# Kernel optimization log

Measured on AMD Instinct MI355X. Metric: run time of the kernel, lower is better.

The kernel has to match this reference:

```python
import jax, jax.numpy as jnp
import numpy as np

B = 2048          # batch
E = 32            # number of expert FCs (len(out_features_nested))
IN = 2048         # in_features
OUT = 1024        # out_features (uniform across experts)


def setup_inputs() -> dict:
    key = jax.random.key(0)
    k1, k2, k3, k4 = jax.random.split(key, 4)
    features = jax.random.normal(k1, (B, IN), dtype=jnp.float32)
    activated = jax.random.normal(k2, (B, E), dtype=jnp.float32)
    # Stacked per-expert Linear params: W[e] is [OUT, IN], b[e] is [OUT]
    W = jax.random.normal(k3, (E, OUT, IN), dtype=jnp.float32) * (1.0 / np.sqrt(IN))
    b = jax.random.normal(k4, (E, OUT), dtype=jnp.float32) * 0.01
    return {"features": features, "W": W, "b": b, "activated": activated, "top_k": 4}


def reference(features, W, b, activated, top_k):
    # Original: parent_indices = activated.argsort(dim=1)[:, :top_k]  (ascending!)
    idx = jnp.argsort(activated, axis=1)[:, :top_k]            # [B, K] int
    # Dense all-expert compute (grouped GEMM), then per-sample gather of the
    # top_k selected experts' outputs. Equivalent math to per-sample Linear calls.
    all_out = jnp.einsum('bi,eoi->beo', features, W) + b        # [B, E, OUT]
    out = jnp.take_along_axis(all_out, idx[:, :, None], axis=1)  # [B, K, OUT]
    return out
```

## Files before the change

kernel.cpp:

```cpp
#include <hip/hip_runtime.h>
#include <hip/hip_bf16.h>
#include <stdint.h>

#define B_N     2048
#define E_N     32
#define IN_N    2048
#define OUT_N   1024
#define TOPK    4

#define BM      256
#define BN      256
#define BK      32
#define NT      (OUT_N / BN)
#define NKT     (IN_N / BK)
#define THREADS 512
#define MAX_SLOTS 64
#define GRID_GEMM (MAX_SLOTS * NT)

#define WS_COUNTS 0
#define WS_NSLOTS 32
#define WS_DESC   64
#define WS_LISTS  256

typedef float  f32x4  __attribute__((ext_vector_type(4)));
typedef __bf16 bf16x8 __attribute__((ext_vector_type(8)));

union Pack8 { bf16x8 v; uint4 u; };

__device__ __forceinline__ uint4 pack8(f32x4 lo, f32x4 hi) {
  Pack8 p;
#pragma unroll
  for (int j = 0; j < 4; ++j) { p.v[j] = (__bf16)lo[j]; p.v[j + 4] = (__bf16)hi[j]; }
  return p.u;
}
__device__ __forceinline__ bf16x8 as_frag(uint4 u) { Pack8 p; p.u = u; return p.v; }

__global__ void k_zero(int* __restrict__ ws) {
  if (threadIdx.x < 64) ws[threadIdx.x] = 0;
}

__global__ void k_topk(const float* __restrict__ act, int* __restrict__ ws) {
  int b = blockIdx.x * blockDim.x + threadIdx.x;
  if (b >= B_N) return;
  float v[E_N];
  const float* a = act + (size_t)b * E_N;
#pragma unroll
  for (int e = 0; e < E_N; ++e) v[e] = a[e];
  unsigned chosen = 0;
#pragma unroll
  for (int k = 0; k < TOPK; ++k) {
    float mv = 3.4e38f; int mi = 0;
#pragma unroll
    for (int e = 0; e < E_N; ++e) {
      bool sel = (((chosen >> e) & 1u) == 0u) && (v[e] < mv);
      mv = sel ? v[e] : mv;
      mi = sel ? e : mi;
    }
    chosen |= (1u << mi);
    int pos = atomicAdd(&ws[WS_COUNTS + mi], 1);
    ws[WS_LISTS + mi * B_N + pos] = (b << 2) | k;
  }
}

__global__ void k_tiles(int* __restrict__ ws) {
  int e = threadIdx.x;
  int c = (e < E_N) ? ws[WS_COUNTS + e] : 0;
  int t = (c + BM - 1) / BM;
  int off = 0, tot = 0;
  for (int j = 0; j < E_N; ++j) {
    int tj = __shfl(t, j, 64);
    if (j < e) off += tj;
    tot += tj;
  }
  if (e < E_N) {
    for (int i = 0; i < t; ++i) ws[WS_DESC + off + i] = (e << 6) | i;
  }
  if (e == 0) ws[WS_NSLOTS] = tot;
}

__global__ __launch_bounds__(THREADS, 2)
void k_gemm(const float* __restrict__ feat, const float* __restrict__ Wm,
            const float* __restrict__ bias, const int* __restrict__ ws,
            float* __restrict__ out) {
  int p = blockIdx.x;
  int x = p & 7, j = p >> 3;
  int slot = x + 8 * (j >> 2);
  int nt   = j & 3;
  if (slot >= ws[WS_NSLOTS]) return;
  int desc = ws[WS_DESC + slot];
  int e = desc >> 6, mt = desc & 63;
  int count = ws[WS_COUNTS + e];
  int m0 = mt * BM;

  __shared__ uint4 lds4[4096];
  __shared__ int gids[BM];

  int tid  = threadIdx.x;
  int lane = tid & 63;
  int wv   = tid >> 6;
  int wm   = wv >> 2;
  int wn   = wv & 3;

  int seg  = tid & 3;
  int ar0  = tid >> 2;
  int ar1  = 128 + (tid >> 2);
  int gid0 = -1, gid1 = -1;
  if (m0 + ar0 < count) gid0 = ws[WS_LISTS + e * B_N + m0 + ar0];
  if (m0 + ar1 < count) gid1 = ws[WS_LISTS + e * B_N + m0 + ar1];
  if (seg == 0) { gids[ar0] = gid0; gids[ar1] = gid1; }
  const float* aptr0 = feat + (size_t)(gid0 >> 2) * IN_N + seg * 8;
  const float* aptr1 = feat + (size_t)(gid1 >> 2) * IN_N + seg * 8;
  int a_wi0 = ar0 * 4 + (seg ^ ((ar0 >> 1) & 3));
  int a_wi1 = ar1 * 4 + (seg ^ ((ar1 >> 1) & 3));

  int wr0 = tid >> 2, wr1 = 128 + (tid >> 2);
  const float* wptr0 = Wm + ((size_t)e * OUT_N + (size_t)(nt * BN + wr0)) * IN_N + seg * 8;
  const float* wptr1 = Wm + ((size_t)e * OUT_N + (size_t)(nt * BN + wr1)) * IN_N + seg * 8;
  int w_wi0 = 1024 + wr0 * 4 + (seg ^ ((wr0 >> 1) & 3));
  int w_wi1 = 1024 + wr1 * 4 + (seg ^ ((wr1 >> 1) & 3));

  int aidx[8], bidx[4];
#pragma unroll
  for (int mi = 0; mi < 8; ++mi) {
    int r = wm * 128 + mi * 16 + (lane & 15);
    aidx[mi] = r * 4 + ((lane >> 4) ^ ((r >> 1) & 3));
  }
#pragma unroll
  for (int ni = 0; ni < 4; ++ni) {
    int r = wn * 64 + ni * 16 + (lane & 15);
    bidx[ni] = 1024 + r * 4 + ((lane >> 4) ^ ((r >> 1) & 3));
  }

  f32x4 ra[4], rw[4];
  const f32x4 zero4 = {0.f, 0.f, 0.f, 0.f};

#define LOAD_TILE(K0)                                                        \
  do {                                                                       \
    if (gid0 >= 0) {                                                         \
      ra[0] = *(const f32x4*)(aptr0 + (K0));                                 \
      ra[1] = *(const f32x4*)(aptr0 + (K0) + 4);                             \
    } else { ra[0] = zero4; ra[1] = zero4; }                                 \
    if (gid1 >= 0) {                                                         \
      ra[2] = *(const f32x4*)(aptr1 + (K0));                                 \
      ra[3] = *(const f32x4*)(aptr1 + (K0) + 4);                             \
    } else { ra[2] = zero4; ra[3] = zero4; }                                 \
    rw[0] = *(const f32x4*)(wptr0 + (K0));                                   \
    rw[1] = *(const f32x4*)(wptr0 + (K0) + 4);                               \
    rw[2] = *(const f32x4*)(wptr1 + (K0));                                   \
    rw[3] = *(const f32x4*)(wptr1 + (K0) + 4);                               \
  } while (0)

#define WRITE_TILE(BUF)                                                      \
  do {                                                                       \
    lds4[(BUF) * 2048 + a_wi0] = pack8(ra[0], ra[1]);                        \
    lds4[(BUF) * 2048 + a_wi1] = pack8(ra[2], ra[3]);                        \
    lds4[(BUF) * 2048 + w_wi0] = pack8(rw[0], rw[1]);                        \
    lds4[(BUF) * 2048 + w_wi1] = pack8(rw[2], rw[3]);                        \
  } while (0)

  f32x4 acc[8][4] = {};

  LOAD_TILE(0);
  WRITE_TILE(0);
  __syncthreads();

  int cur = 0;
#pragma unroll 1
  for (int kt = 0; kt < NKT; ++kt) {
    bool pf = (kt + 1 < NKT);
    if (pf) LOAD_TILE((kt + 1) * BK);

    int base = cur * 2048;
    bf16x8 af[8], bfr[4];
#pragma unroll
    for (int mi = 0; mi < 8; ++mi) af[mi] = as_frag(lds4[base + aidx[mi]]);
#pragma unroll
    for (int ni = 0; ni < 4; ++ni) bfr[ni] = as_frag(lds4[base + bidx[ni]]);
#pragma unroll
    for (int mi = 0; mi < 8; ++mi)
#pragma unroll
      for (int ni = 0; ni < 4; ++ni)
        acc[mi][ni] = __builtin_amdgcn_mfma_f32_16x16x32_bf16(af[mi], bfr[ni], acc[mi][ni], 0, 0, 0);

    if (pf) WRITE_TILE(cur ^ 1);
    __syncthreads();
    cur ^= 1;
  }

#pragma unroll
  for (int ni = 0; ni < 4; ++ni) {
    int col = nt * BN + wn * 64 + ni * 16 + (lane & 15);
    float bs = bias[e * OUT_N + col];
#pragma unroll
    for (int mi = 0; mi < 8; ++mi) {
#pragma unroll
      for (int j2 = 0; j2 < 4; ++j2) {
        int g = gids[wm * 128 + mi * 16 + (lane >> 4) * 4 + j2];
        if (g >= 0) out[(size_t)g * OUT_N + col] = acc[mi][ni][j2] + bs;
      }
    }
  }
}

extern "C" void kernel_launch(void* const* d_in, const int* in_sizes, int n_in,
                              void* d_out, int out_size, void* d_ws, size_t ws_size,
                              hipStream_t stream) {
  const float* feat = (const float*)d_in[0];
  const float* Wm   = (const float*)d_in[1];
  const float* bias = (const float*)d_in[2];
  const float* act  = (const float*)d_in[3];
  int*   ws  = (int*)d_ws;
  float* out = (float*)d_out;

  hipLaunchKernelGGL(k_zero,  dim3(1),          dim3(64),      0, stream, ws);
  hipLaunchKernelGGL(k_topk,  dim3(B_N / 256),  dim3(256),     0, stream, act, ws);
  hipLaunchKernelGGL(k_tiles, dim3(1),          dim3(64),      0, stream, ws);
  hipLaunchKernelGGL(k_gemm,  dim3(GRID_GEMM),  dim3(THREADS), 0, stream,
                     feat, Wm, bias, ws, out);
}
```

Baseline: 154.7 us.

## Pre-convert features to bf16 and stream A tiles directly into LDS

Adds a pre-pass that converts the feature matrix to bf16 in workspace. The gathered A rows are then loaded straight into LDS with global_load_lds, which removes the register round-trip and the fp32-to-bf16 packing from the inner loop. The K loop becomes a two-step unrolled pipeline with a triple-buffered A tile, double-buffered W registers, and explicit vmcnt waits instead of __syncthreads. The cost is an extra conversion kernel and its traffic, a larger LDS footprint, and the fragility of hand-placed waitcnt and barrier ordering.

```diff
diff --git a/kernel.cpp b/kernel.cpp
--- a/kernel.cpp
+++ b/kernel.cpp
@@ -21,6 +21,7 @@
 #define WS_NSLOTS 32
 #define WS_DESC   64
 #define WS_LISTS  256
+#define FEATB_OFF 264192
 
 typedef float  f32x4  __attribute__((ext_vector_type(4)));
 typedef __bf16 bf16x8 __attribute__((ext_vector_type(8)));
@@ -35,8 +36,21 @@
 }
 __device__ __forceinline__ bf16x8 as_frag(uint4 u) { Pack8 p; p.u = u; return p.v; }
 
+__device__ __forceinline__ void glds16(const void* g, const uint4* l) {
+  __builtin_amdgcn_global_load_lds(
+      (const __attribute__((address_space(1))) void*)g,
+      (__attribute__((address_space(3))) void*)l, 16, 0, 0);
+}
+
 __global__ void k_zero(int* __restrict__ ws) {
   if (threadIdx.x < 64) ws[threadIdx.x] = 0;
+}
+
+__global__ void k_conv(const float* __restrict__ f, unsigned short* __restrict__ o) {
+  int i = (blockIdx.x * 256 + threadIdx.x) * 8;
+  f32x4 a = *(const f32x4*)(f + i);
+  f32x4 b = *(const f32x4*)(f + i + 4);
+  *(uint4*)(o + i) = pack8(a, b);
 }
 
 __global__ void k_topk(const float* __restrict__ act, int* __restrict__ ws) {
@@ -79,7 +93,7 @@
 }
 
 __global__ __launch_bounds__(THREADS, 2)
-void k_gemm(const float* __restrict__ feat, const float* __restrict__ Wm,
+void k_gemm(const unsigned short* __restrict__ featb, const float* __restrict__ Wm,
             const float* __restrict__ bias, const int* __restrict__ ws,
             float* __restrict__ out) {
   int p = blockIdx.x;
@@ -92,8 +106,7 @@
   int count = ws[WS_COUNTS + e];
   int m0 = mt * BM;
 
-  __shared__ uint4 lds4[4096];
-  __shared__ int gids[BM];
+  __shared__ uint4 lds4[5120];
 
   int tid  = threadIdx.x;
   int lane = tid & 63;
@@ -101,23 +114,22 @@
   int wm   = wv >> 2;
   int wn   = wv & 3;
 
-  int seg  = tid & 3;
-  int ar0  = tid >> 2;
-  int ar1  = 128 + (tid >> 2);
-  int gid0 = -1, gid1 = -1;
-  if (m0 + ar0 < count) gid0 = ws[WS_LISTS + e * B_N + m0 + ar0];
-  if (m0 + ar1 < count) gid1 = ws[WS_LISTS + e * B_N + m0 + ar1];
-  if (seg == 0) { gids[ar0] = gid0; gids[ar1] = gid1; }
-  const float* aptr0 = feat + (size_t)(gid0 >> 2) * IN_N + seg * 8;
-  const float* aptr1 = feat + (size_t)(gid1 >> 2) * IN_N + seg * 8;
-  int a_wi0 = ar0 * 4 + (seg ^ ((ar0 >> 1) & 3));
-  int a_wi1 = ar1 * 4 + (seg ^ ((ar1 >> 1) & 3));
-
-  int wr0 = tid >> 2, wr1 = 128 + (tid >> 2);
-  const float* wptr0 = Wm + ((size_t)e * OUT_N + (size_t)(nt * BN + wr0)) * IN_N + seg * 8;
-  const float* wptr1 = Wm + ((size_t)e * OUT_N + (size_t)(nt * BN + wr1)) * IN_N + seg * 8;
-  int w_wi0 = 1024 + wr0 * 4 + (seg ^ ((wr0 >> 1) & 3));
-  int w_wi1 = 1024 + wr1 * 4 + (seg ^ ((wr1 >> 1) & 3));
+  const unsigned short* asrc0;
+  const unsigned short* asrc1;
+  {
+    int s0 = wv * 128 + lane,      r0 = s0 >> 2, t0 = s0 & 3;
+    int s1 = wv * 128 + 64 + lane, r1 = s1 >> 2, t1 = s1 & 3;
+    int g0 = (m0 + r0 < count) ? (ws[WS_LISTS + e * B_N + m0 + r0] >> 2) : 0;
+    int g1 = (m0 + r1 < count) ? (ws[WS_LISTS + e * B_N + m0 + r1] >> 2) : 0;
+    asrc0 = featb + (size_t)g0 * IN_N + ((t0 ^ ((r0 >> 1) & 3)) * 8);
+    asrc1 = featb + (size_t)g1 * IN_N + ((t1 ^ ((r1 >> 1) & 3)) * 8);
+  }
+
+  int wrow = tid >> 1, half = tid & 1;
+  const float* wp = Wm + ((size_t)e * OUT_N + (size_t)(nt * BN + wrow)) * IN_N + half * 16;
+  int wswz = (wrow >> 1) & 3;
+  int wsl0 = wrow * 4 + ((half * 2) ^ wswz);
+  int wsl1 = wrow * 4 + ((half * 2 + 1) ^ wswz);
 
   int aidx[8], bidx[4];
 #pragma unroll
@@ -128,64 +140,94 @@
 #pragma unroll
   for (int ni = 0; ni < 4; ++ni) {
     int r = wn * 64 + ni * 16 + (lane & 15);
-    bidx[ni] = 1024 + r * 4 + ((lane >> 4) ^ ((r >> 1) & 3));
-  }
-
-  f32x4 ra[4], rw[4];
-  const f32x4 zero4 = {0.f, 0.f, 0.f, 0.f};
-
-#define LOAD_TILE(K0)                                                        \
-  do {                                                                       \
-    if (gid0 >= 0) {                                                         \
-      ra[0] = *(const f32x4*)(aptr0 + (K0));                                 \
-      ra[1] = *(const f32x4*)(aptr0 + (K0) + 4);                             \
-    } else { ra[0] = zero4; ra[1] = zero4; }                                 \
-    if (gid1 >= 0) {                                                         \
-      ra[2] = *(const f32x4*)(aptr1 + (K0));                                 \
-      ra[3] = *(const f32x4*)(aptr1 + (K0) + 4);                             \
-    } else { ra[2] = zero4; ra[3] = zero4; }                                 \
-    rw[0] = *(const f32x4*)(wptr0 + (K0));                                   \
-    rw[1] = *(const f32x4*)(wptr0 + (K0) + 4);                               \
-    rw[2] = *(const f32x4*)(wptr1 + (K0));                                   \
-    rw[3] = *(const f32x4*)(wptr1 + (K0) + 4);                               \
-  } while (0)
-
-#define WRITE_TILE(BUF)                                                      \
-  do {                                                                       \
-    lds4[(BUF) * 2048 + a_wi0] = pack8(ra[0], ra[1]);                        \
-    lds4[(BUF) * 2048 + a_wi1] = pack8(ra[2], ra[3]);                        \
-    lds4[(BUF) * 2048 + w_wi0] = pack8(rw[0], rw[1]);                        \
-    lds4[(BUF) * 2048 + w_wi1] = pack8(rw[2], rw[3]);                        \
-  } while (0)
-
+    bidx[ni] = r * 4 + ((lane >> 4) ^ ((r >> 1) & 3));
+  }
+
+  f32x4 rwA[4], rwB[4];
   f32x4 acc[8][4] = {};
 
-  LOAD_TILE(0);
-  WRITE_TILE(0);
-  __syncthreads();
-
-  int cur = 0;
+#define AGLDS(K2, AB)                                                         \
+  do {                                                                        \
+    glds16(asrc0 + (size_t)(K2) * BK, &lds4[(AB) * 1024 + wv * 128]);         \
+    glds16(asrc1 + (size_t)(K2) * BK, &lds4[(AB) * 1024 + wv * 128 + 64]);    \
+  } while (0)
+
+#define WLOAD(K2, RW)                                                         \
+  do {                                                                        \
+    RW[0] = *(const f32x4*)(wp + (size_t)(K2) * BK);                          \
+    RW[1] = *(const f32x4*)(wp + (size_t)(K2) * BK + 4);                      \
+    RW[2] = *(const f32x4*)(wp + (size_t)(K2) * BK + 8);                      \
+    RW[3] = *(const f32x4*)(wp + (size_t)(K2) * BK + 12);                     \
+  } while (0)
+
+#define WPACK(RW, WB)                                                         \
+  do {                                                                        \
+    lds4[3072 + (WB) * 1024 + wsl0] = pack8(RW[0], RW[1]);                    \
+    lds4[3072 + (WB) * 1024 + wsl1] = pack8(RW[2], RW[3]);                    \
+  } while (0)
+
+#define MFMAS(AB, WB)                                                         \
+  do {                                                                        \
+    bf16x8 af[8], bfr[4];                                                     \
+    _Pragma("unroll")                                                         \
+    for (int ni = 0; ni < 4; ++ni)                                            \
+      bfr[ni] = as_frag(lds4[3072 + (WB) * 1024 + bidx[ni]]);                 \
+    _Pragma("unroll")                                                         \
+    for (int mi = 0; mi < 8; ++mi) af[mi] = as_frag(lds4[(AB) * 1024 + aidx[mi]]); \
+    _Pragma("unroll")                                                         \
+    for (int mi = 0; mi < 8; ++mi)                                            \
+      _Pragma("unroll")                                                       \
+      for (int ni = 0; ni < 4; ++ni)                                          \
+        acc[mi][ni] = __builtin_amdgcn_mfma_f32_16x16x32_bf16(af[mi], bfr[ni], acc[mi][ni], 0, 0, 0); \
+  } while (0)
+
+#define WAITVM(N)                                                             \
+  asm volatile("s_waitcnt vmcnt(" #N ")" ::: "memory");                       \
+  __builtin_amdgcn_sched_barrier(0)
+
+#define BARRIER()                                                             \
+  asm volatile("s_waitcnt lgkmcnt(0)" ::: "memory");                          \
+  __builtin_amdgcn_sched_barrier(0);                                          \
+  __builtin_amdgcn_s_barrier()
+
+  AGLDS(0, 0);
+  AGLDS(1, 1);
+  WLOAD(0, rwA);
+  WLOAD(1, rwB);
+  WAITVM(4);
+  WPACK(rwA, 0);
+  BARRIER();
+
+  int ab = 0;
 #pragma unroll 1
-  for (int kt = 0; kt < NKT; ++kt) {
-    bool pf = (kt + 1 < NKT);
-    if (pf) LOAD_TILE((kt + 1) * BK);
-
-    int base = cur * 2048;
-    bf16x8 af[8], bfr[4];
-#pragma unroll
-    for (int mi = 0; mi < 8; ++mi) af[mi] = as_frag(lds4[base + aidx[mi]]);
-#pragma unroll
-    for (int ni = 0; ni < 4; ++ni) bfr[ni] = as_frag(lds4[base + bidx[ni]]);
-#pragma unroll
-    for (int mi = 0; mi < 8; ++mi)
-#pragma unroll
-      for (int ni = 0; ni < 4; ++ni)
-        acc[mi][ni] = __builtin_amdgcn_mfma_f32_16x16x32_bf16(af[mi], bfr[ni], acc[mi][ni], 0, 0, 0);
-
-    if (pf) WRITE_TILE(cur ^ 1);
-    __syncthreads();
-    cur ^= 1;
-  }
+  for (int kt = 0; kt < NKT - 2; kt += 2) {
+    {
+      int ab2 = (ab == 0) ? 2 : ab - 1;
+      AGLDS(kt + 2, ab2);
+      WLOAD(kt + 2, rwA);
+      MFMAS(ab, 0);
+      WAITVM(6);
+      WPACK(rwB, 1);
+      BARRIER();
+    }
+    {
+      int abo = (ab == 2) ? 0 : ab + 1;
+      int ab2 = (abo == 0) ? 2 : abo - 1;
+      AGLDS(kt + 3, ab2);
+      WLOAD(kt + 3, rwB);
+      MFMAS(abo, 1);
+      WAITVM(6);
+      WPACK(rwA, 0);
+      BARRIER();
+    }
+    ab = (ab == 1) ? 0 : ((ab == 2) ? 1 : 2);
+  }
+
+  MFMAS(2, 0);
+  WAITVM(0);
+  WPACK(rwB, 1);
+  BARRIER();
+  MFMAS(0, 1);
 
 #pragma unroll
   for (int ni = 0; ni < 4; ++ni) {
@@ -195,8 +237,11 @@
     for (int mi = 0; mi < 8; ++mi) {
 #pragma unroll
       for (int j2 = 0; j2 < 4; ++j2) {
-        int g = gids[wm * 128 + mi * 16 + (lane >> 4) * 4 + j2];
-        if (g >= 0) out[(size_t)g * OUT_N + col] = acc[mi][ni][j2] + bs;
+        int row = wm * 128 + mi * 16 + (lane >> 4) * 4 + j2;
+        if (m0 + row < count) {
+          int g = ws[WS_LISTS + e * B_N + m0 + row];
+          out[(size_t)g * OUT_N + col] = acc[mi][ni][j2] + bs;
+        }
       }
     }
   }
@@ -210,11 +255,13 @@
   const float* bias = (const float*)d_in[2];
   const float* act  = (const float*)d_in[3];
   int*   ws  = (int*)d_ws;
+  unsigned short* featb = (unsigned short*)((char*)d_ws + FEATB_OFF);
   float* out = (float*)d_out;
 
-  hipLaunchKernelGGL(k_zero,  dim3(1),          dim3(64),      0, stream, ws);
-  hipLaunchKernelGGL(k_topk,  dim3(B_N / 256),  dim3(256),     0, stream, act, ws);
-  hipLaunchKernelGGL(k_tiles, dim3(1),          dim3(64),      0, stream, ws);
-  hipLaunchKernelGGL(k_gemm,  dim3(GRID_GEMM),  dim3(THREADS), 0, stream,
-                     feat, Wm, bias, ws, out);
-}
+  hipLaunchKernelGGL(k_zero,  dim3(1),                  dim3(64),      0, stream, ws);
+  hipLaunchKernelGGL(k_conv,  dim3(B_N * IN_N / 2048),  dim3(256),     0, stream, feat, featb);
+  hipLaunchKernelGGL(k_topk,  dim3(B_N / 256),          dim3(256),     0, stream, act, ws);
+  hipLaunchKernelGGL(k_tiles, dim3(1),                  dim3(64),      0, stream, ws);
+  hipLaunchKernelGGL(k_gemm,  dim3(GRID_GEMM),          dim3(THREADS), 0, stream,
+                     featb, Wm, bias, ws, out);
+}
```

New measurement: 159.8 us. 1.03x slower.
